# Optimization experiments

Hardware: AMD Instinct MI355X
Metric: run time of the kernel (lower is better)

## Reference

```python
import jax, jax.numpy as jnp
import numpy as np

N_HEADS = 12


def setup_inputs() -> dict:
    key = jax.random.key(0)
    k1, k2, k3 = jax.random.split(key, 3)
    B, W, C = 2, 2048, 768
    in_sequence_bwc = jax.random.normal(k1, (B, W, C), dtype=jnp.float32)
    # QKV projection weight [3C, C] (torch Linear convention: out_features x in_features)
    w_attn = jax.random.normal(k2, (3 * C, C), dtype=jnp.float32) * (1.0 / np.sqrt(C))
    w_proj = jax.random.normal(k3, (C, C), dtype=jnp.float32) * (1.0 / np.sqrt(C))
    return {"in_sequence_bwc": in_sequence_bwc, "w_attn": w_attn, "w_proj": w_proj}


def reference(in_sequence_bwc, w_attn, w_proj):
    B, W, C = in_sequence_bwc.shape
    H = N_HEADS
    K = C // H  # head dim
    qkv = jnp.einsum('bwc,dc->bwd', in_sequence_bwc, w_attn)  # [B,W,3C]
    q, k, v = jnp.split(qkv, 3, axis=-1)
    # [B,H,W,K]
    q = q.reshape(B, W, H, K).transpose(0, 2, 1, 3)
    k = k.reshape(B, W, H, K).transpose(0, 2, 1, 3)
    v = v.reshape(B, W, H, K).transpose(0, 2, 1, 3)
    scores = jnp.einsum('bhqk,bhsk->bhqs', q, k) / jnp.sqrt(jnp.float32(K))
    causal = jnp.tril(jnp.ones((W, W), dtype=bool))
    scores = jnp.where(causal[None, None], scores, jnp.float32(-jnp.inf))
    probs = jax.nn.softmax(scores, axis=-1)
    out = jnp.einsum('bhqs,bhsk->bhqk', probs, v)  # [B,H,W,K]
    out = out.transpose(0, 2, 1, 3).reshape(B, W, C)
    return jnp.einsum('bwc,dc->bwd', out, w_proj)
```

## Files before the change

kernel.cpp:

```cpp
#include <hip/hip_runtime.h>

constexpr int B_  = 2;
constexpr int W_  = 2048;
constexpr int C_  = 768;
constexpr int H_  = 12;
constexpr int HD  = 64;
constexpr int C3  = 3 * C_;
constexpr int M_  = B_ * W_;
constexpr int NSLOT = 80;

typedef float  f32x4 __attribute__((ext_vector_type(4)));
typedef short  s16x8 __attribute__((ext_vector_type(8)));
typedef short  s16x4 __attribute__((ext_vector_type(4)));
typedef unsigned short u16;
typedef unsigned int   u32;

__device__ __forceinline__ u16 f2bf(float f) {
    unsigned int u = __float_as_uint(f);
    u += 0x7FFFu + ((u >> 16) & 1u);
    return (u16)(u >> 16);
}

__device__ __forceinline__ void gload_lds16(const u16* g, u16* l) {
    __builtin_amdgcn_global_load_lds(
        (const __attribute__((address_space(1))) unsigned int*)g,
        (__attribute__((address_space(3))) unsigned int*)l, 16, 0, 0);
}

__global__ __launch_bounds__(256)
void cvt_all(const float* __restrict__ x, const float* __restrict__ wa,
             const float* __restrict__ wp, u16* __restrict__ xb,
             u16* __restrict__ wab, u16* __restrict__ wpb)
{
    const int n0 = M_ * C_ / 8;
    const int n1 = n0 + C3 * C_ / 8;
    const int n2 = n1 + C_ * C_ / 8;
    int i = blockIdx.x * 256 + threadIdx.x;
    const float* s; u16* d; int j;
    if (i < n0)      { s = x;  d = xb;  j = i; }
    else if (i < n1) { s = wa; d = wab; j = i - n0; }
    else if (i < n2) { s = wp; d = wpb; j = i - n1; }
    else return;
    const float4 a = reinterpret_cast<const float4*>(s)[j * 2];
    const float4 b = reinterpret_cast<const float4*>(s)[j * 2 + 1];
    s16x8 v;
    v[0] = (short)f2bf(a.x); v[1] = (short)f2bf(a.y);
    v[2] = (short)f2bf(a.z); v[3] = (short)f2bf(a.w);
    v[4] = (short)f2bf(b.x); v[5] = (short)f2bf(b.y);
    v[6] = (short)f2bf(b.z); v[7] = (short)f2bf(b.w);
    reinterpret_cast<s16x8*>(d)[j] = v;
}

__device__ __forceinline__ void store_out(u16*  p, float v) { *p = f2bf(v); }
__device__ __forceinline__ void store_out(float* p, float v) { *p = v; }

template <typename OutT>
__global__ __launch_bounds__(256)
void gemm_nt_mfma(const u16* __restrict__ A, const u16* __restrict__ Bm,
                  OutT* __restrict__ Y, int Ndim, int Kdim)
{
    __shared__ __align__(16) u16 As[128 * 64];
    __shared__ __align__(16) u16 Bs[128 * 64];

    const int t  = threadIdx.x;
    const int w  = t >> 6;
    const int l  = t & 63;
    const int lg = l >> 4;
    const int ln = l & 15;
    const int wm = w >> 1;
    const int wn = w & 1;
    const int m0 = blockIdx.x * 128;
    const int n0 = blockIdx.y * 128;

    f32x4 acc[4][4];
    #pragma unroll
    for (int mi = 0; mi < 4; ++mi)
        #pragma unroll
        for (int ni = 0; ni < 4; ++ni)
            acc[mi][ni] = (f32x4){0.f, 0.f, 0.f, 0.f};

    for (int k0 = 0; k0 < Kdim; k0 += 64) {
        #pragma unroll
        for (int it = 0; it < 4; ++it) {
            const int c  = t + it * 256;
            const int fr = c >> 7;
            const int s  = (c >> 6) & 1;
            const int kc = (c >> 4) & 3;
            const int rr = c & 15;
            const size_t koff = (size_t)k0 + s * 32 + kc * 8;
            const u16* ga = A  + (size_t)(m0 + fr * 16 + rr) * Kdim + koff;
            const u16* gb = Bm + (size_t)(n0 + fr * 16 + rr) * Kdim + koff;
            gload_lds16(ga, &As[(size_t)(it * 256 + w * 64) * 8]);
            gload_lds16(gb, &Bs[(size_t)(it * 256 + w * 64) * 8]);
        }
        __syncthreads();

        #pragma unroll
        for (int s = 0; s < 2; ++s) {
            s16x8 af[4], bf[4];
            #pragma unroll
            for (int mi = 0; mi < 4; ++mi)
                af[mi] = *reinterpret_cast<const s16x8*>(
                    &As[(size_t)((wm * 4 + mi) * 128 + s * 64 + lg * 16 + ln) * 8]);
            #pragma unroll
            for (int ni = 0; ni < 4; ++ni)
                bf[ni] = *reinterpret_cast<const s16x8*>(
                    &Bs[(size_t)((wn * 4 + ni) * 128 + s * 64 + lg * 16 + ln) * 8]);
            __builtin_amdgcn_s_setprio(1);
            #pragma unroll
            for (int mi = 0; mi < 4; ++mi)
                #pragma unroll
                for (int ni = 0; ni < 4; ++ni)
                    acc[mi][ni] = __builtin_amdgcn_mfma_f32_16x16x32_bf16(
                        af[mi], bf[ni], acc[mi][ni], 0, 0, 0);
            __builtin_amdgcn_s_setprio(0);
        }
        __syncthreads();
    }

    #pragma unroll
    for (int mi = 0; mi < 4; ++mi) {
        const int row = m0 + wm * 64 + mi * 16 + lg * 4;
        #pragma unroll
        for (int ni = 0; ni < 4; ++ni) {
            const int col = n0 + wn * 64 + ni * 16 + ln;
            #pragma unroll
            for (int r = 0; r < 4; ++r)
                store_out(&Y[(size_t)(row + r) * Ndim + col], acc[mi][ni][r]);
        }
    }
}

__global__ __launch_bounds__(256)
void attn_partial(const u16* __restrict__ qkv, float* __restrict__ po,
                  float* __restrict__ pl)
{
    __shared__ __align__(16) unsigned char KsB[64 * 128];
    __shared__ __align__(16) unsigned char VtB[64 * 144];

    const int t  = threadIdx.x;
    const int w  = t >> 6;
    const int l  = t & 63;
    const int lg = l >> 4;
    const int ln = l & 15;
    const int p  = blockIdx.x;
    const int h  = blockIdx.y;
    const int b  = blockIdx.z;

    int qt, ck;
    if (p < 8)       { qt = p;                 ck = 0; }
    else if (p < 24) { qt = 8  + ((p - 8) >> 1);  ck = (p - 8) & 1; }
    else if (p < 48) { qt = 16 + (p - 24) / 3;    ck = (p - 24) % 3; }
    else             { qt = 24 + ((p - 48) >> 2); ck = (p - 48) & 3; }

    const int qb  = qt * 64;
    const int q0w = qb + w * 16;
    const int g0  = ck * 8;
    const int g1  = min(qt + 1, g0 + 8);
    const int slot = (b * H_ + h) * NSLOT + p;

    const u16* base  = qkv + (size_t)(b * W_) * C3;
    const u16* kbase = base + C_ + h * HD;
    const u16* vbase = base + 2 * C_ + h * HD;

    s16x8 qf[2];
    {
        const u16* qrow = base + (size_t)(q0w + ln) * C3 + h * HD;
        #pragma unroll
        for (int kc = 0; kc < 2; ++kc)
            qf[kc] = *reinterpret_cast<const s16x8*>(&qrow[kc * 32 + lg * 8]);
    }

    s16x8 onesf;
    {
        const short v1 = (ln == 0) ? (short)0x3F80 : (short)0;
        #pragma unroll
        for (int i = 0; i < 8; ++i) onesf[i] = v1;
    }

    f32x4 o[4];
    #pragma unroll
    for (int i = 0; i < 4; ++i) o[i] = (f32x4){0.f, 0.f, 0.f, 0.f};
    f32x4 o4 = (f32x4){0.f, 0.f, 0.f, 0.f};

    const float c1 = 0.18033688011112042f;
    const float c2 = 17.312340490667562f;

    const int sk_kc  = (t >> 6) & 1;
    const int sk_lgS = (t >> 4) & 3;
    const int sk_lnS = t & 15;
    const int sk_kg0 = t >> 7;
    const size_t sk_off = (size_t)(sk_kg0 * 16 + sk_lnS) * C3
                        + sk_kc * 32 + sk_lgS * 8;
    const bool vstage = (t < 128);
    const int vrun = (t >> 4) & 7;
    const int vK0  = (vrun >> 2) * 32 + (vrun & 3) * 4;
    const int vdq  = (t & 15) * 4;
    const int kfb  = l * 16;

    s16x8 kr[2];
    s16x4 vr[8];

    {
        const int s0 = g0 * 64;
        const u16* ks = kbase + (size_t)s0 * C3 + sk_off;
        kr[0] = *reinterpret_cast<const s16x8*>(ks);
        kr[1] = *reinterpret_cast<const s16x8*>(ks + (size_t)32 * C3);
        if (vstage) {
            const u16* vsrc = vbase + (size_t)(s0 + vK0) * C3 + vdq;
            #pragma unroll
            for (int e = 0; e < 8; ++e)
                vr[e] = *reinterpret_cast<const s16x4*>(
                    &vsrc[(size_t)((e >> 2) * 16 + (e & 3)) * C3]);
        }
    }

    for (int g = g0; g < g1; ++g) {
        const int s0 = g * 64;

        __syncthreads();

        *reinterpret_cast<s16x8*>(KsB + t * 16)         = kr[0];
        *reinterpret_cast<s16x8*>(KsB + (t + 256) * 16) = kr[1];
        if (vstage) {
            #pragma unroll
            for (int j = 0; j < 4; ++j) {
                s16x8 pk = { vr[0][j], vr[1][j], vr[2][j], vr[3][j],
                             vr[4][j], vr[5][j], vr[6][j], vr[7][j] };
                *reinterpret_cast<s16x8*>(
                    VtB + (vdq + j) * 144 + vrun * 16) = pk;
            }
        }

        if (g + 1 < g1) {
            const int s1 = s0 + 64;
            const u16* ks = kbase + (size_t)s1 * C3 + sk_off;
            kr[0] = *reinterpret_cast<const s16x8*>(ks);
            kr[1] = *reinterpret_cast<const s16x8*>(ks + (size_t)32 * C3);
            if (vstage) {
                const u16* vsrc = vbase + (size_t)(s1 + vK0) * C3 + vdq;
                #pragma unroll
                for (int e = 0; e < 8; ++e)
                    vr[e] = *reinterpret_cast<const s16x4*>(
                        &vsrc[(size_t)((e >> 2) * 16 + (e & 3)) * C3]);
            }
        }

        __syncthreads();

        #pragma unroll
        for (int c = 0; c < 2; ++c) {
            if (s0 + c * 32 <= q0w + 15) {
                float pt[2][4];
                #pragma unroll
                for (int n2 = 0; n2 < 2; ++n2) {
                    const unsigned char* kfrag = KsB + (c * 2 + n2) * 2048 + kfb;
                    s16x8 kf0 = *reinterpret_cast<const s16x8*>(kfrag);
                    s16x8 kf1 = *reinterpret_cast<const s16x8*>(kfrag + 1024);
                    f32x4 s = (f32x4){0.f, 0.f, 0.f, 0.f};
                    __builtin_amdgcn_s_setprio(1);
                    s = __builtin_amdgcn_mfma_f32_16x16x32_bf16(kf0, qf[0], s, 0, 0, 0);
                    s = __builtin_amdgcn_mfma_f32_16x16x32_bf16(kf1, qf[1], s, 0, 0, 0);
                    __builtin_amdgcn_s_setprio(0);
                    const int kg0   = s0 + c * 32 + n2 * 16 + lg * 4;
                    const int klast = s0 + c * 32 + n2 * 16 + 15;
                    if (klast <= q0w) {
                        #pragma unroll
                        for (int r = 0; r < 4; ++r)
                            pt[n2][r] = exp2f(fmaf(s[r], c1, -c2));
                    } else {
                        const int qg = q0w + ln;
                        #pragma unroll
                        for (int r = 0; r < 4; ++r)
                            pt[n2][r] = (kg0 + r <= qg)
                                      ? exp2f(fmaf(s[r], c1, -c2)) : 0.0f;
                    }
                }
                union { s16x8 v; u32 wd[4]; } afu;
                asm("v_cvt_pk_bf16_f32 %0, %1, %2"
                    : "=v"(afu.wd[0]) : "v"(pt[0][0]), "v"(pt[0][1]));
                asm("v_cvt_pk_bf16_f32 %0, %1, %2"
                    : "=v"(afu.wd[1]) : "v"(pt[0][2]), "v"(pt[0][3]));
                asm("v_cvt_pk_bf16_f32 %0, %1, %2"
                    : "=v"(afu.wd[2]) : "v"(pt[1][0]), "v"(pt[1][1]));
                asm("v_cvt_pk_bf16_f32 %0, %1, %2"
                    : "=v"(afu.wd[3]) : "v"(pt[1][2]), "v"(pt[1][3]));
                const s16x8 af = afu.v;
                s16x8 vf[4];
                #pragma unroll
                for (int dt = 0; dt < 4; ++dt)
                    vf[dt] = *reinterpret_cast<const s16x8*>(
                        VtB + (dt * 16 + ln) * 144 + c * 64 + lg * 16);
                __builtin_amdgcn_s_setprio(1);
                #pragma unroll
                for (int dt = 0; dt < 4; ++dt)
                    o[dt] = __builtin_amdgcn_mfma_f32_16x16x32_bf16(af, vf[dt], o[dt], 0, 0, 0);
                o4 = __builtin_amdgcn_mfma_f32_16x16x32_bf16(af, onesf, o4, 0, 0, 0);
                __builtin_amdgcn_s_setprio(0);
            }
        }
    }

    if (ln == 0) {
        #pragma unroll
        for (int r = 0; r < 4; ++r)
            pl[(size_t)slot * 64 + w * 16 + lg * 4 + r] = o4[r];
    }
    float* os = po + (size_t)slot * 4096;
    #pragma unroll
    for (int r = 0; r < 4; ++r)
        #pragma unroll
        for (int dt = 0; dt < 4; ++dt)
            os[(w * 16 + lg * 4 + r) * 64 + dt * 16 + ln] = o[dt][r];
}

__global__ __launch_bounds__(256)
void attn_combine(const float* __restrict__ po, const float* __restrict__ pl,
                  u16* __restrict__ aob)
{
    const int qt = blockIdx.x;
    const int h  = blockIdx.y;
    const int b  = blockIdx.z;
    const int nc = (qt + 8) >> 3;
    int cum;
    if (qt < 8)       cum = qt;
    else if (qt < 16) cum = 8  + 2 * (qt - 8);
    else if (qt < 24) cum = 24 + 3 * (qt - 16);
    else              cum = 48 + 4 * (qt - 24);
    const int slot0 = (b * H_ + h) * NSLOT + cum;

    const int tid = threadIdx.x;
    const int i   = tid >> 2;
    const int d0  = (tid & 3) * 16;

    f32x4 acc[4] = { (f32x4){0,0,0,0}, (f32x4){0,0,0,0},
                     (f32x4){0,0,0,0}, (f32x4){0,0,0,0} };
    float lt = 0.0f;
    for (int c = 0; c < nc; ++c) {
        const float* os = po + (size_t)(slot0 + c) * 4096 + i * 64 + d0;
        #pragma unroll
        for (int v = 0; v < 4; ++v)
            acc[v] += *reinterpret_cast<const f32x4*>(os + v * 4);
        lt += pl[(size_t)(slot0 + c) * 64 + i];
    }
    const float inv = 1.0f / lt;

    u16* dst = aob + (size_t)(b * W_ + qt * 64 + i) * C_ + h * HD + d0;
    s16x8 ov[2];
    #pragma unroll
    for (int v = 0; v < 4; ++v)
        #pragma unroll
        for (int e = 0; e < 4; ++e)
            ov[v >> 1][(v & 1) * 4 + e] = (short)f2bf(acc[v][e] * inv);
    *reinterpret_cast<s16x8*>(dst)     = ov[0];
    *reinterpret_cast<s16x8*>(dst + 8) = ov[1];
}

extern "C" void kernel_launch(void* const* d_in, const int* in_sizes, int n_in,
                              void* d_out, int out_size, void* d_ws, size_t ws_size,
                              hipStream_t stream)
{
    const float* x      = (const float*)d_in[0];
    const float* w_attn = (const float*)d_in[1];
    const float* w_proj = (const float*)d_in[2];
    float* out = (float*)d_out;

    u16* xb   = (u16*)d_ws;
    u16* wab  = xb   + (size_t)M_ * C_;
    u16* wpb  = wab  + (size_t)C3 * C_;
    u16* qkvb = wpb  + (size_t)C_ * C_;
    u16* aob  = qkvb + (size_t)M_ * C3;
    float* po = (float*)(aob + (size_t)M_ * C_);
    float* pl = po + (size_t)B_ * H_ * NSLOT * 4096;

    {
        const int total8 = (M_ * C_ + C3 * C_ + C_ * C_) / 8;
        cvt_all<<<(total8 + 255) / 256, 256, 0, stream>>>(
            x, w_attn, w_proj, xb, wab, wpb);
    }

    {
        dim3 grid(M_ / 128, C3 / 128);
        gemm_nt_mfma<u16><<<grid, 256, 0, stream>>>(xb, wab, qkvb, C3, C_);
    }

    {
        dim3 grid(NSLOT, H_, B_);
        attn_partial<<<grid, 256, 0, stream>>>(qkvb, po, pl);
    }
    {
        dim3 grid(W_ / 64, H_, B_);
        attn_combine<<<grid, 256, 0, stream>>>(po, pl, aob);
    }

    {
        dim3 grid(M_ / 128, C_ / 128);
        gemm_nt_mfma<float><<<grid, 256, 0, stream>>>(aob, wpb, out, C_, C_);
    }
}
```

Baseline: 124.6 us.

## Double-buffer LDS tiles in GEMM to overlap global loads with MFMA

New measurement: 126.2 us. No clear change (+1.3%).

```diff
diff --git a/kernel.cpp b/kernel.cpp
--- a/kernel.cpp
+++ b/kernel.cpp
@@ -59,8 +59,8 @@
 void gemm_nt_mfma(const u16* __restrict__ A, const u16* __restrict__ Bm,
                   OutT* __restrict__ Y, int Ndim, int Kdim)
 {
-    __shared__ __align__(16) u16 As[128 * 64];
-    __shared__ __align__(16) u16 Bs[128 * 64];
+    __shared__ __align__(16) u16 As[2][128 * 64];
+    __shared__ __align__(16) u16 Bs[2][128 * 64];
 
     const int t  = threadIdx.x;
     const int w  = t >> 6;
@@ -79,21 +79,27 @@
         for (int ni = 0; ni < 4; ++ni)
             acc[mi][ni] = (f32x4){0.f, 0.f, 0.f, 0.f};
 
+    #define GEMM_STAGE(buf, k0s)                                              \
+        _Pragma("unroll")                                                     \
+        for (int it = 0; it < 4; ++it) {                                      \
+            const int c  = t + it * 256;                                      \
+            const int fr = c >> 7;                                            \
+            const int s  = (c >> 6) & 1;                                      \
+            const int kc = (c >> 4) & 3;                                      \
+            const int rr = c & 15;                                            \
+            const size_t koff = (size_t)(k0s) + s * 32 + kc * 8;              \
+            gload_lds16(A  + (size_t)(m0 + fr * 16 + rr) * Kdim + koff,       \
+                        &As[buf][(size_t)(it * 256 + w * 64) * 8]);           \
+            gload_lds16(Bm + (size_t)(n0 + fr * 16 + rr) * Kdim + koff,       \
+                        &Bs[buf][(size_t)(it * 256 + w * 64) * 8]);           \
+        }
+
+    GEMM_STAGE(0, 0)
+    __syncthreads();
+
+    int cur = 0;
     for (int k0 = 0; k0 < Kdim; k0 += 64) {
-        #pragma unroll
-        for (int it = 0; it < 4; ++it) {
-            const int c  = t + it * 256;
-            const int fr = c >> 7;
-            const int s  = (c >> 6) & 1;
-            const int kc = (c >> 4) & 3;
-            const int rr = c & 15;
-            const size_t koff = (size_t)k0 + s * 32 + kc * 8;
-            const u16* ga = A  + (size_t)(m0 + fr * 16 + rr) * Kdim + koff;
-            const u16* gb = Bm + (size_t)(n0 + fr * 16 + rr) * Kdim + koff;
-            gload_lds16(ga, &As[(size_t)(it * 256 + w * 64) * 8]);
-            gload_lds16(gb, &Bs[(size_t)(it * 256 + w * 64) * 8]);
-        }
-        __syncthreads();
+        if (k0 + 64 < Kdim) { GEMM_STAGE(cur ^ 1, k0 + 64) }
 
         #pragma unroll
         for (int s = 0; s < 2; ++s) {
@@ -101,11 +107,11 @@
             #pragma unroll
             for (int mi = 0; mi < 4; ++mi)
                 af[mi] = *reinterpret_cast<const s16x8*>(
-                    &As[(size_t)((wm * 4 + mi) * 128 + s * 64 + lg * 16 + ln) * 8]);
+                    &As[cur][(size_t)((wm * 4 + mi) * 128 + s * 64 + lg * 16 + ln) * 8]);
             #pragma unroll
             for (int ni = 0; ni < 4; ++ni)
                 bf[ni] = *reinterpret_cast<const s16x8*>(
-                    &Bs[(size_t)((wn * 4 + ni) * 128 + s * 64 + lg * 16 + ln) * 8]);
+                    &Bs[cur][(size_t)((wn * 4 + ni) * 128 + s * 64 + lg * 16 + ln) * 8]);
             __builtin_amdgcn_s_setprio(1);
             #pragma unroll
             for (int mi = 0; mi < 4; ++mi)
@@ -115,8 +121,11 @@
                         af[mi], bf[ni], acc[mi][ni], 0, 0, 0);
             __builtin_amdgcn_s_setprio(0);
         }
+
         __syncthreads();
-    }
+        cur ^= 1;
+    }
+    #undef GEMM_STAGE
 
     #pragma unroll
     for (int mi = 0; mi < 4; ++mi) {
@@ -186,12 +195,8 @@
     const float c1 = 0.18033688011112042f;
     const float c2 = 17.312340490667562f;
 
-    const int sk_kc  = (t >> 6) & 1;
-    const int sk_lgS = (t >> 4) & 3;
-    const int sk_lnS = t & 15;
-    const int sk_kg0 = t >> 7;
-    const size_t sk_off = (size_t)(sk_kg0 * 16 + sk_lnS) * C3
-                        + sk_kc * 32 + sk_lgS * 8;
+    const size_t sk_off = (size_t)((t >> 7) * 16 + (t & 15)) * C3
+                        + ((t >> 6) & 1) * 32 + ((t >> 4) & 3) * 8;
     const bool vstage = (t < 128);
     const int vrun = (t >> 4) & 7;
     const int vK0  = (vrun >> 2) * 32 + (vrun & 3) * 4;
```
